# Performance work log

Measured on AMD Instinct MI355X. Metric: run time of the kernel, lower is better.

The kernel has to match this reference:

```python
import jax, jax.numpy as jnp
import numpy as np

DIM = 1024          # n_embd
NUM_EXPERTS = 8
TOP_K = 2
HIDDEN = 4 * DIM // TOP_K   # expert_hidden_dim = 2048
BS, SLEN = 1, 2048


def setup_inputs() -> dict:
    key = jax.random.key(0)
    k0, k1, k2, k3 = jax.random.split(key, 4)
    x = jax.random.normal(k0, (BS, SLEN, DIM), dtype=jnp.float32)
    gate_w = jax.random.normal(k1, (NUM_EXPERTS, DIM), dtype=jnp.float32) * 0.02
    w_up = jax.random.normal(k2, (NUM_EXPERTS, HIDDEN, DIM), dtype=jnp.float32) * 0.02
    w_down = jax.random.normal(k3, (NUM_EXPERTS, DIM, HIDDEN), dtype=jnp.float32) * 0.02
    expert_bias = jnp.zeros((NUM_EXPERTS,), dtype=jnp.float32)
    return {"x": x, "gate_w": gate_w, "w_up": w_up, "w_down": w_down,
            "expert_bias": expert_bias}


def _moe(x, gate_w, w_up, w_down, expert_bias):
    bs, slen, dim = x.shape
    xf = x.reshape(-1, dim)                       # (T, D)
    # Sigmoid router (scores in fp32, bias only affects selection, not weights)
    scores = jax.nn.sigmoid(xf @ gate_w.T)        # (T, E)
    biased = scores + expert_bias
    _, sel = jax.lax.top_k(biased, TOP_K)         # (T, K) expert ids, distinct per token
    top_scores = jnp.take_along_axis(scores, sel, axis=-1)  # (T, K)

    # Scatter/gather dispatch + grouped GEMM is mathematically equivalent to:
    #   out[t] = sum_k W_down[e_tk] @ relu(W_up[e_tk] @ (s_tk * x[t]))^2
    # Loop over the small fixed expert set via lax.scan; unassigned tokens
    # contribute exactly zero (relu(0)^2 = 0), honoring the routing sparsity.
    def body(acc, ew):
        e, wu, wd = ew
        # combined routing weight for this expert per token (at most one slot)
        w_t = jnp.sum(jnp.where(sel == e, top_scores, 0.0), axis=-1)  # (T,)
        xe = xf * w_t[:, None]                    # (T, D), zero for non-routed
        h = jnp.square(jax.nn.relu(xe @ wu.T))    # (T, H)  relu(x)^2 activation
        return acc + h @ wd.T, None

    out0 = jnp.zeros_like(xf)
    out, _ = jax.lax.scan(body, out0, (jnp.arange(NUM_EXPERTS), w_up, w_down))
    return out.reshape(bs, slen, dim)


def reference(x, gate_w, w_up, w_down, expert_bias):
    return _moe(x, gate_w, w_up, w_down, expert_bias)
```

## Files before the change

### kernel.cpp

```cpp
#include <hip/hip_runtime.h>
#include <cstdint>
#include <cstddef>

#define T_TOK 2048
#define DMODEL 1024
#define NEXP 8
#define HID 2048
#define DUMP_ID 4096

typedef __bf16 bf16x8 __attribute__((ext_vector_type(8)));
typedef float f32x4 __attribute__((ext_vector_type(4)));
typedef unsigned short u16;
typedef u16 u16x8 __attribute__((ext_vector_type(8)));

__device__ __forceinline__ u16 f2bf(float f) {
    union { float f; unsigned int u; } v; v.f = f;
    unsigned int u = v.u;
    unsigned int r = (u + 0x7FFFu + ((u >> 16) & 1u)) >> 16;
    return (u16)r;
}

__device__ __forceinline__ void gl2lds16(const void* g, void* l) {
    __builtin_amdgcn_global_load_lds(
        (const __attribute__((address_space(1))) void*)g,
        (__attribute__((address_space(3))) void*)l,
        16, 0, 0);
}

__global__ __launch_bounds__(256) void fused_pre(
    const float4* __restrict__ x4, const float4* __restrict__ gw4,
    const float* __restrict__ bias, ushort4* __restrict__ xb4,
    unsigned int* __restrict__ selpack, float* __restrict__ w2,
    unsigned int* __restrict__ xb_dump_row_u32) {
    const int b = blockIdx.x;
    const int tid = threadIdx.x;

    if (b == 256) {
        if (tid < DMODEL / 2) xb_dump_row_u32[tid] = 0;
        return;
    }
    const int wv = tid >> 6;
    const int lane = tid & 63;
    const int pair = b * 4 + wv;
    const int t0 = 2 * pair, t1 = t0 + 1;

    float acc0[NEXP], acc1[NEXP];
#pragma unroll
    for (int e = 0; e < NEXP; ++e) { acc0[e] = 0.f; acc1[e] = 0.f; }
#pragma unroll
    for (int j = 0; j < 4; ++j) {
        int i4 = lane + j * 64;
        float4 a0 = x4[t0 * 256 + i4];
        float4 a1 = x4[t1 * 256 + i4];
        ushort4 s0, s1;
        s0.x = f2bf(a0.x); s0.y = f2bf(a0.y); s0.z = f2bf(a0.z); s0.w = f2bf(a0.w);
        s1.x = f2bf(a1.x); s1.y = f2bf(a1.y); s1.z = f2bf(a1.z); s1.w = f2bf(a1.w);
        xb4[t0 * 256 + i4] = s0;
        xb4[t1 * 256 + i4] = s1;
#pragma unroll
        for (int e = 0; e < NEXP; ++e) {
            float4 g = gw4[e * 256 + i4];
            acc0[e] += a0.x * g.x + a0.y * g.y + a0.z * g.z + a0.w * g.w;
            acc1[e] += a1.x * g.x + a1.y * g.y + a1.z * g.z + a1.w * g.w;
        }
    }
#pragma unroll
    for (int e = 0; e < NEXP; ++e)
        for (int off = 32; off > 0; off >>= 1) {
            acc0[e] += __shfl_xor(acc0[e], off, 64);
            acc1[e] += __shfl_xor(acc1[e], off, 64);
        }
    if (lane == 0) {
#pragma unroll
        for (int tt = 0; tt < 2; ++tt) {
            int t = tt ? t1 : t0;
            float sc[NEXP], bi[NEXP];
#pragma unroll
            for (int e = 0; e < NEXP; ++e) {
                float a = tt ? acc1[e] : acc0[e];
                sc[e] = 1.f / (1.f + expf(-a));
                bi[e] = sc[e] + bias[e];
            }
            int e0 = 0;
            for (int e = 1; e < NEXP; ++e) if (bi[e] > bi[e0]) e0 = e;
            int e1 = -1;
            for (int e = 0; e < NEXP; ++e) {
                if (e == e0) continue;
                if (e1 < 0 || bi[e] > bi[e1]) e1 = e;
            }
            selpack[t] = (unsigned int)e0 | ((unsigned int)e1 << 8);
            w2[2 * t]     = sc[e0] * sc[e0];
            w2[2 * t + 1] = sc[e1] * sc[e1];
        }
    }
}

__global__ __launch_bounds__(256) void build_lists(
    const unsigned int* __restrict__ selpack, int* __restrict__ counts,
    int* __restrict__ list) {
    const int e = blockIdx.x;
    const int tid = threadIdx.x;
    const int lane = tid & 63;
    const int wv = tid >> 6;
    __shared__ int wsum[4];
    __shared__ int base;
    if (tid == 0) base = 0;
    __syncthreads();
    for (int tb = 0; tb < T_TOK; tb += 256) {
        int t = tb + tid;
        unsigned int sp = selpack[t];
        bool f1 = ((sp >> 8) & 255u) == (unsigned)e;
        bool f = ((sp & 255u) == (unsigned)e) | f1;
        int id = 2 * t + (f1 ? 1 : 0);
        unsigned long long m = __ballot(f);
        int pos = __popcll(m & ((1ull << lane) - 1ull));
        if (lane == 0) wsum[wv] = __popcll(m);
        __syncthreads();
        int woff = 0;
#pragma unroll
        for (int i = 0; i < 4; ++i) if (i < wv) woff += wsum[i];
        int bse = base;
        if (f) list[e * T_TOK + bse + woff + pos] = id;
        __syncthreads();
        if (tid == 0) base = bse + wsum[0] + wsum[1] + wsum[2] + wsum[3];
    }
    __syncthreads();
    int total = base;
    if (tid == 0) counts[e] = total;
    for (int i = total + tid; i < T_TOK; i += 256) list[e * T_TOK + i] = DUMP_ID;
}

template <int MODE>
__global__ __launch_bounds__(256, 2) void moe_gemm(
    const u16* __restrict__ Asrc, const int* __restrict__ list,
    const int* __restrict__ counts, const float* __restrict__ Ball32,
    const float* __restrict__ w2, u16* __restrict__ Hout,
    float* __restrict__ Pout) {
    constexpr int K   = (MODE == 0) ? DMODEL : HID;
    constexpr int NKT = K / 64;
    constexpr int NTN = ((MODE == 0) ? HID : DMODEL) / 128;
    constexpr int LOGNTN = (MODE == 0) ? 4 : 3;

    const int b = blockIdx.x;
    const int e = b & 7;
    const int rest = b >> 3;
    const int m0 = (rest >> LOGNTN) * 128;
    if (m0 >= counts[e]) return;
    const int n0 = (rest & (NTN - 1)) * 128;

    const int tid = threadIdx.x;
    const int lane = tid & 63;
    const int w = tid >> 6;

    __shared__ u16 As[128 * 64];
    __shared__ u16 Bs[128 * 64];

    const int* mylist = list + e * T_TOK + m0;
    const float* B32 = Ball32 + (size_t)e * HID * DMODEL;

    const u16* ap[4];
    const float4* bp[4];
    int bwr[4];
    const int c8 = tid & 7;
#pragma unroll
    for (int it = 0; it < 4; ++it) {
        int row = it * 32 + (tid >> 3);
        int gs = c8 ^ (row & 7);
        if (MODE == 0) {
            int id = mylist[row];
            ap[it] = Asrc + (size_t)(id >> 1) * K + gs * 8;
        } else {
            ap[it] = Asrc + (size_t)(e * T_TOK + m0 + row) * K + gs * 8;
        }
        bp[it] = (const float4*)(B32 + (size_t)(n0 + row) * K) + c8 * 2;
        bwr[it] = row * 64 + gs * 8;
    }

    const int wm = (w >> 1) * 64;
    const int wn = (w & 1) * 64;
    const int quad = lane >> 4;
    const int lrow = lane & 15;

    f32x4 acc[4][4];
#pragma unroll
    for (int i = 0; i < 4; ++i)
#pragma unroll
        for (int j = 0; j < 4; ++j) acc[i][j] = f32x4{0.f, 0.f, 0.f, 0.f};

    for (int kt = 0; kt < NKT; ++kt) {
#pragma unroll
        for (int it = 0; it < 4; ++it)
            gl2lds16(ap[it] + kt * 64, &As[(it * 256 + w * 64) * 8]);
        float4 bu[4][2];
#pragma unroll
        for (int it = 0; it < 4; ++it) {
            bu[it][0] = bp[it][kt * 16];
            bu[it][1] = bp[it][kt * 16 + 1];
        }
#pragma unroll
        for (int it = 0; it < 4; ++it) {
            u16x8 o;
            o[0] = f2bf(bu[it][0].x); o[1] = f2bf(bu[it][0].y);
            o[2] = f2bf(bu[it][0].z); o[3] = f2bf(bu[it][0].w);
            o[4] = f2bf(bu[it][1].x); o[5] = f2bf(bu[it][1].y);
            o[6] = f2bf(bu[it][1].z); o[7] = f2bf(bu[it][1].w);
            *(u16x8*)&Bs[bwr[it]] = o;
        }
        __syncthreads();
#pragma unroll
        for (int s = 0; s < 2; ++s) {
            const int q = s * 4 + quad;
            bf16x8 af[4], bfr[4];
#pragma unroll
            for (int i = 0; i < 4; ++i) {
                int ra = wm + i * 16 + lrow;
                int rb = wn + i * 16 + lrow;
                af[i]  = *(const bf16x8*)&As[ra * 64 + (q ^ (ra & 7)) * 8];
                bfr[i] = *(const bf16x8*)&Bs[rb * 64 + (q ^ (rb & 7)) * 8];
            }
#pragma unroll
            for (int i = 0; i < 4; ++i)
#pragma unroll
                for (int j = 0; j < 4; ++j)
                    acc[i][j] = __builtin_amdgcn_mfma_f32_16x16x32_bf16(
                        af[i], bfr[j], acc[i][j], 0, 0, 0);
        }
        __syncthreads();
    }

#pragma unroll
    for (int i = 0; i < 4; ++i) {
        int mbase = wm + i * 16 + (lane >> 4) * 4;
        int ids[4];
        float ww[4];
#pragma unroll
        for (int r = 0; r < 4; ++r) {
            ids[r] = mylist[mbase + r];
            if (MODE == 0) ww[r] = w2[ids[r]];
        }
#pragma unroll
        for (int j = 0; j < 4; ++j) {
            int n = n0 + wn + j * 16 + (lane & 15);
#pragma unroll
            for (int r = 0; r < 4; ++r) {
                float v = acc[i][j][r];
                if (MODE == 0) {
                    v = (v > 0.f) ? v * v * ww[r] : 0.f;
                    Hout[(size_t)(e * T_TOK + m0 + mbase + r) * HID + n] = f2bf(v);
                } else {
                    if (ids[r] != DUMP_ID)
                        Pout[(size_t)ids[r] * DMODEL + n] = v;
                }
            }
        }
    }
}

__global__ __launch_bounds__(256) void combine(
    const float4* __restrict__ part4, float4* __restrict__ out4) {
    int idx = blockIdx.x * 256 + threadIdx.x;
    int t = idx >> 8;
    int d4 = idx & 255;
    float4 p0 = part4[(size_t)(2 * t) * 256 + d4];
    float4 p1 = part4[(size_t)(2 * t + 1) * 256 + d4];
    float4 o;
    o.x = p0.x + p1.x; o.y = p0.y + p1.y;
    o.z = p0.z + p1.z; o.w = p0.w + p1.w;
    out4[idx] = o;
}

extern "C" void kernel_launch(void* const* d_in, const int* in_sizes, int n_in,
                              void* d_out, int out_size, void* d_ws, size_t ws_size,
                              hipStream_t stream) {
    const float* x      = (const float*)d_in[0];
    const float* gate_w = (const float*)d_in[1];
    const float* w_up   = (const float*)d_in[2];
    const float* w_down = (const float*)d_in[3];
    const float* bias   = (const float*)d_in[4];
    float* out = (float*)d_out;

    char* p = (char*)d_ws;
    int* counts = (int*)p;                 p += 256;
    int* list   = (int*)p;                 p += NEXP * T_TOK * 4;
    float* w2   = (float*)p;               p += 4104 * 4;
    unsigned int* selpack = (unsigned int*)p;  p += T_TOK * 4;
    u16* xb  = (u16*)p;  p += (size_t)(T_TOK + 1) * DMODEL * 2;
    u16* h   = (u16*)p;  p += (size_t)NEXP * T_TOK * HID * 2;
    float* part = (float*)p;  p += (size_t)2 * T_TOK * DMODEL * 4;

    fused_pre<<<257, 256, 0, stream>>>(
        (const float4*)x, (const float4*)gate_w, bias,
        (ushort4*)xb, selpack, w2,
        (unsigned int*)(xb + (size_t)T_TOK * DMODEL));

    build_lists<<<NEXP, 256, 0, stream>>>(selpack, counts, list);

    moe_gemm<0><<<16 * (HID / 128) * NEXP, 256, 0, stream>>>(
        xb, list, counts, w_up, w2, h, nullptr);

    moe_gemm<1><<<16 * (DMODEL / 128) * NEXP, 256, 0, stream>>>(
        h, list, counts, w_down, w2, nullptr, part);

    combine<<<T_TOK * DMODEL / 4 / 256, 256, 0, stream>>>(
        (const float4*)part, (float4*)out);
}
```

Before: 255.0 us.

## Software-pipeline grouped GEMM K-loop with multi-buffered LDS and register prefetch

Restructures the expert GEMM main loop into a two-stage-ahead software pipeline. A tiles go into a triple-buffered LDS ring via direct global-to-LDS loads, and B tiles are prefetched into alternating register sets before being converted to bf16 into double-buffered LDS. Explicit vmcnt waits and one barrier per step replace the two syncthreads per iteration. The goal is to hide global load latency behind the MFMA work, at the cost of more LDS (80KB) and more registers, which may lower occupancy.

```diff
diff --git a/kernel.cpp b/kernel.cpp
--- a/kernel.cpp
+++ b/kernel.cpp
@@ -26,6 +26,14 @@
         (__attribute__((address_space(3))) void*)l,
         16, 0, 0);
 }
+
+#define WAITV(N) asm volatile("s_waitcnt vmcnt(" #N ")" ::: "memory")
+#define LGKM0_BAR()                                            \
+    do {                                                       \
+        asm volatile("s_waitcnt lgkmcnt(0)" ::: "memory");     \
+        __builtin_amdgcn_s_barrier();                          \
+        __builtin_amdgcn_sched_barrier(0);                     \
+    } while (0)
 
 __global__ __launch_bounds__(256) void fused_pre(
     const float4* __restrict__ x4, const float4* __restrict__ gw4,
@@ -152,8 +160,8 @@
     const int lane = tid & 63;
     const int w = tid >> 6;
 
-    __shared__ u16 As[128 * 64];
-    __shared__ u16 Bs[128 * 64];
+    __shared__ u16 As[3][128 * 64];
+    __shared__ u16 Bs[2][128 * 64];
 
     const int* mylist = list + e * T_TOK + m0;
     const float* B32 = Ball32 + (size_t)e * HID * DMODEL;
@@ -187,26 +195,42 @@
 #pragma unroll
         for (int j = 0; j < 4; ++j) acc[i][j] = f32x4{0.f, 0.f, 0.f, 0.f};
 
-    for (int kt = 0; kt < NKT; ++kt) {
-#pragma unroll
-        for (int it = 0; it < 4; ++it)
-            gl2lds16(ap[it] + kt * 64, &As[(it * 256 + w * 64) * 8]);
-        float4 bu[4][2];
-#pragma unroll
-        for (int it = 0; it < 4; ++it) {
-            bu[it][0] = bp[it][kt * 16];
-            bu[it][1] = bp[it][kt * 16 + 1];
-        }
-#pragma unroll
-        for (int it = 0; it < 4; ++it) {
-            u16x8 o;
-            o[0] = f2bf(bu[it][0].x); o[1] = f2bf(bu[it][0].y);
-            o[2] = f2bf(bu[it][0].z); o[3] = f2bf(bu[it][0].w);
-            o[4] = f2bf(bu[it][1].x); o[5] = f2bf(bu[it][1].y);
-            o[6] = f2bf(bu[it][1].z); o[7] = f2bf(bu[it][1].w);
-            *(u16x8*)&Bs[bwr[it]] = o;
-        }
-        __syncthreads();
+    float4 buE[4][2], buO[4][2];
+
+#define ISSUE_A(KT)                                                          \
+    do {                                                                     \
+        u16* dst_ = &As[(KT) % 3][0];                                        \
+        _Pragma("unroll")                                                    \
+        for (int it_ = 0; it_ < 4; ++it_)                                    \
+            gl2lds16(ap[it_] + (KT) * 64, dst_ + (it_ * 256 + w * 64) * 8);  \
+    } while (0)
+
+#define LOAD_B(KT, BU)                                                       \
+    do {                                                                     \
+        _Pragma("unroll")                                                    \
+        for (int it_ = 0; it_ < 4; ++it_) {                                  \
+            BU[it_][0] = bp[it_][(KT) * 16];                                 \
+            BU[it_][1] = bp[it_][(KT) * 16 + 1];                             \
+        }                                                                    \
+    } while (0)
+
+#define WRITE_B(KT, BU)                                                      \
+    do {                                                                     \
+        u16* dst_ = &Bs[(KT) & 1][0];                                        \
+        _Pragma("unroll")                                                    \
+        for (int it_ = 0; it_ < 4; ++it_) {                                  \
+            u16x8 o_;                                                        \
+            o_[0] = f2bf(BU[it_][0].x); o_[1] = f2bf(BU[it_][0].y);          \
+            o_[2] = f2bf(BU[it_][0].z); o_[3] = f2bf(BU[it_][0].w);          \
+            o_[4] = f2bf(BU[it_][1].x); o_[5] = f2bf(BU[it_][1].y);          \
+            o_[6] = f2bf(BU[it_][1].z); o_[7] = f2bf(BU[it_][1].w);          \
+            *(u16x8*)(dst_ + bwr[it_]) = o_;                                 \
+        }                                                                    \
+    } while (0)
+
+    auto compute = [&](int kt) {
+        const u16* As_ = &As[kt % 3][0];
+        const u16* Bs_ = &Bs[kt & 1][0];
 #pragma unroll
         for (int s = 0; s < 2; ++s) {
             const int q = s * 4 + quad;
@@ -215,8 +239,8 @@
             for (int i = 0; i < 4; ++i) {
                 int ra = wm + i * 16 + lrow;
                 int rb = wn + i * 16 + lrow;
-                af[i]  = *(const bf16x8*)&As[ra * 64 + (q ^ (ra & 7)) * 8];
-                bfr[i] = *(const bf16x8*)&Bs[rb * 64 + (q ^ (rb & 7)) * 8];
+                af[i]  = *(const bf16x8*)(As_ + ra * 64 + (q ^ (ra & 7)) * 8);
+                bfr[i] = *(const bf16x8*)(Bs_ + rb * 64 + (q ^ (rb & 7)) * 8);
             }
 #pragma unroll
             for (int i = 0; i < 4; ++i)
@@ -225,8 +249,40 @@
                     acc[i][j] = __builtin_amdgcn_mfma_f32_16x16x32_bf16(
                         af[i], bfr[j], acc[i][j], 0, 0, 0);
         }
-        __syncthreads();
-    }
+    };
+
+    LOAD_B(0, buE);
+    ISSUE_A(0);
+    LOAD_B(1, buO);
+    ISSUE_A(1);
+    WAITV(12);
+    WRITE_B(0, buE);
+    LGKM0_BAR();
+
+    for (int kt = 0; kt < NKT; kt += 2) {
+        {
+            const bool i2 = (kt + 2 < NKT);
+            if (i2) { LOAD_B(kt + 2, buE); ISSUE_A(kt + 2); }
+            compute(kt);
+            if (i2) WAITV(16); else WAITV(4);
+            WRITE_B(kt + 1, buO);
+            if (i2) WAITV(12); else WAITV(0);
+            LGKM0_BAR();
+        }
+        {
+            const int k1 = kt + 1;
+            const bool i2 = (k1 + 2 < NKT);
+            if (i2) { LOAD_B(k1 + 2, buO); ISSUE_A(k1 + 2); }
+            compute(k1);
+            if (i2) WAITV(16); else WAITV(4);
+            if (k1 + 1 < NKT) WRITE_B(k1 + 1, buE);
+            if (i2) WAITV(12); else WAITV(0);
+            LGKM0_BAR();
+        }
+    }
+#undef ISSUE_A
+#undef LOAD_B
+#undef WRITE_B
 
 #pragma unroll
     for (int i = 0; i < 4; ++i) {
```

Measured after the change: 266.8 us. +4.6%, slower.

## Fuse all MoE stages into one persistent kernel with grid barriers

Applied to the files above, without the earlier changes.

Replaces the five separate launches (router/convert, list build, up GEMM, down GEMM, combine) with a single persistent kernel of 512 blocks. The stages are separated by atomic-counter grid barriers, and each GEMM stage loops over its tiles. This removes per-launch overhead and gaps between kernels. In exchange it adds a memset launch, spin-wait barriers, and reliance on all 512 blocks being co-resident. The static tile striding may also balance GEMM work less well than a full hardware-scheduled grid.

```diff
diff --git a/kernel.cpp b/kernel.cpp
--- a/kernel.cpp
+++ b/kernel.cpp
@@ -7,6 +7,7 @@
 #define NEXP 8
 #define HID 2048
 #define DUMP_ID 4096
+#define NBLK 512
 
 typedef __bf16 bf16x8 __attribute__((ext_vector_type(8)));
 typedef float f32x4 __attribute__((ext_vector_type(4)));
@@ -27,123 +28,33 @@
         16, 0, 0);
 }
 
-__global__ __launch_bounds__(256) void fused_pre(
-    const float4* __restrict__ x4, const float4* __restrict__ gw4,
-    const float* __restrict__ bias, ushort4* __restrict__ xb4,
-    unsigned int* __restrict__ selpack, float* __restrict__ w2,
-    unsigned int* __restrict__ xb_dump_row_u32) {
-    const int b = blockIdx.x;
-    const int tid = threadIdx.x;
-
-    if (b == 256) {
-        if (tid < DMODEL / 2) xb_dump_row_u32[tid] = 0;
-        return;
-    }
-    const int wv = tid >> 6;
-    const int lane = tid & 63;
-    const int pair = b * 4 + wv;
-    const int t0 = 2 * pair, t1 = t0 + 1;
-
-    float acc0[NEXP], acc1[NEXP];
-#pragma unroll
-    for (int e = 0; e < NEXP; ++e) { acc0[e] = 0.f; acc1[e] = 0.f; }
-#pragma unroll
-    for (int j = 0; j < 4; ++j) {
-        int i4 = lane + j * 64;
-        float4 a0 = x4[t0 * 256 + i4];
-        float4 a1 = x4[t1 * 256 + i4];
-        ushort4 s0, s1;
-        s0.x = f2bf(a0.x); s0.y = f2bf(a0.y); s0.z = f2bf(a0.z); s0.w = f2bf(a0.w);
-        s1.x = f2bf(a1.x); s1.y = f2bf(a1.y); s1.z = f2bf(a1.z); s1.w = f2bf(a1.w);
-        xb4[t0 * 256 + i4] = s0;
-        xb4[t1 * 256 + i4] = s1;
-#pragma unroll
-        for (int e = 0; e < NEXP; ++e) {
-            float4 g = gw4[e * 256 + i4];
-            acc0[e] += a0.x * g.x + a0.y * g.y + a0.z * g.z + a0.w * g.w;
-            acc1[e] += a1.x * g.x + a1.y * g.y + a1.z * g.z + a1.w * g.w;
-        }
-    }
-#pragma unroll
-    for (int e = 0; e < NEXP; ++e)
-        for (int off = 32; off > 0; off >>= 1) {
-            acc0[e] += __shfl_xor(acc0[e], off, 64);
-            acc1[e] += __shfl_xor(acc1[e], off, 64);
-        }
-    if (lane == 0) {
-#pragma unroll
-        for (int tt = 0; tt < 2; ++tt) {
-            int t = tt ? t1 : t0;
-            float sc[NEXP], bi[NEXP];
-#pragma unroll
-            for (int e = 0; e < NEXP; ++e) {
-                float a = tt ? acc1[e] : acc0[e];
-                sc[e] = 1.f / (1.f + expf(-a));
-                bi[e] = sc[e] + bias[e];
-            }
-            int e0 = 0;
-            for (int e = 1; e < NEXP; ++e) if (bi[e] > bi[e0]) e0 = e;
-            int e1 = -1;
-            for (int e = 0; e < NEXP; ++e) {
-                if (e == e0) continue;
-                if (e1 < 0 || bi[e] > bi[e1]) e1 = e;
-            }
-            selpack[t] = (unsigned int)e0 | ((unsigned int)e1 << 8);
-            w2[2 * t]     = sc[e0] * sc[e0];
-            w2[2 * t + 1] = sc[e1] * sc[e1];
-        }
-    }
-}
-
-__global__ __launch_bounds__(256) void build_lists(
-    const unsigned int* __restrict__ selpack, int* __restrict__ counts,
-    int* __restrict__ list) {
-    const int e = blockIdx.x;
-    const int tid = threadIdx.x;
-    const int lane = tid & 63;
-    const int wv = tid >> 6;
-    __shared__ int wsum[4];
-    __shared__ int base;
-    if (tid == 0) base = 0;
+__device__ __forceinline__ void gbar(int* bar, int idx) {
+    __threadfence();
     __syncthreads();
-    for (int tb = 0; tb < T_TOK; tb += 256) {
-        int t = tb + tid;
-        unsigned int sp = selpack[t];
-        bool f1 = ((sp >> 8) & 255u) == (unsigned)e;
-        bool f = ((sp & 255u) == (unsigned)e) | f1;
-        int id = 2 * t + (f1 ? 1 : 0);
-        unsigned long long m = __ballot(f);
-        int pos = __popcll(m & ((1ull << lane) - 1ull));
-        if (lane == 0) wsum[wv] = __popcll(m);
-        __syncthreads();
-        int woff = 0;
-#pragma unroll
-        for (int i = 0; i < 4; ++i) if (i < wv) woff += wsum[i];
-        int bse = base;
-        if (f) list[e * T_TOK + bse + woff + pos] = id;
-        __syncthreads();
-        if (tid == 0) base = bse + wsum[0] + wsum[1] + wsum[2] + wsum[3];
+    if (threadIdx.x == 0) {
+        atomicAdd(&bar[idx], 1);
+        while (atomicAdd(&bar[idx], 0) < NBLK)
+            __builtin_amdgcn_s_sleep(8);
     }
     __syncthreads();
-    int total = base;
-    if (tid == 0) counts[e] = total;
-    for (int i = total + tid; i < T_TOK; i += 256) list[e * T_TOK + i] = DUMP_ID;
+    __threadfence();
 }
 
 template <int MODE>
-__global__ __launch_bounds__(256, 2) void moe_gemm(
-    const u16* __restrict__ Asrc, const int* __restrict__ list,
-    const int* __restrict__ counts, const float* __restrict__ Ball32,
-    const float* __restrict__ w2, u16* __restrict__ Hout,
-    float* __restrict__ Pout) {
+__device__ void gemm_tile(int tix, const u16* __restrict__ Asrc,
+                          const int* __restrict__ list,
+                          const int* __restrict__ counts,
+                          const float* __restrict__ Ball32,
+                          const float* __restrict__ w2,
+                          u16* __restrict__ Hout, float* __restrict__ Pout,
+                          u16* As, u16* Bs) {
     constexpr int K   = (MODE == 0) ? DMODEL : HID;
     constexpr int NKT = K / 64;
     constexpr int NTN = ((MODE == 0) ? HID : DMODEL) / 128;
     constexpr int LOGNTN = (MODE == 0) ? 4 : 3;
 
-    const int b = blockIdx.x;
-    const int e = b & 7;
-    const int rest = b >> 3;
+    const int e = tix & 7;
+    const int rest = tix >> 3;
     const int m0 = (rest >> LOGNTN) * 128;
     if (m0 >= counts[e]) return;
     const int n0 = (rest & (NTN - 1)) * 128;
@@ -151,9 +62,6 @@
     const int tid = threadIdx.x;
     const int lane = tid & 63;
     const int w = tid >> 6;
-
-    __shared__ u16 As[128 * 64];
-    __shared__ u16 Bs[128 * 64];
 
     const int* mylist = list + e * T_TOK + m0;
     const float* B32 = Ball32 + (size_t)e * HID * DMODEL;
@@ -256,30 +164,151 @@
     }
 }
 
-__global__ __launch_bounds__(256) void combine(
-    const float4* __restrict__ part4, float4* __restrict__ out4) {
-    int idx = blockIdx.x * 256 + threadIdx.x;
-    int t = idx >> 8;
-    int d4 = idx & 255;
-    float4 p0 = part4[(size_t)(2 * t) * 256 + d4];
-    float4 p1 = part4[(size_t)(2 * t + 1) * 256 + d4];
-    float4 o;
-    o.x = p0.x + p1.x; o.y = p0.y + p1.y;
-    o.z = p0.z + p1.z; o.w = p0.w + p1.w;
-    out4[idx] = o;
+__global__ __launch_bounds__(256, 2) void moe_fused(
+    const float4* __restrict__ x4, const float4* __restrict__ gw4,
+    const float* __restrict__ bias,
+    u16* __restrict__ xb, unsigned int* __restrict__ selpack,
+    float* __restrict__ w2, int* __restrict__ counts, int* __restrict__ list,
+    const float* __restrict__ wu32, const float* __restrict__ wd32,
+    u16* __restrict__ h, float* __restrict__ part, float* __restrict__ out,
+    int* __restrict__ bar) {
+    const int b = blockIdx.x;
+    const int tid = threadIdx.x;
+
+    __shared__ u16 As[128 * 64];
+    __shared__ u16 Bs[128 * 64];
+    __shared__ int wsum[4];
+    __shared__ int sbase;
+
+    if (b < 256) {
+        ushort4* xb4 = (ushort4*)xb;
+        const int wv = tid >> 6;
+        const int lane = tid & 63;
+        const int pair = b * 4 + wv;
+        const int t0 = 2 * pair, t1 = t0 + 1;
+
+        float acc0[NEXP], acc1[NEXP];
+#pragma unroll
+        for (int e = 0; e < NEXP; ++e) { acc0[e] = 0.f; acc1[e] = 0.f; }
+#pragma unroll
+        for (int j = 0; j < 4; ++j) {
+            int i4 = lane + j * 64;
+            float4 a0 = x4[t0 * 256 + i4];
+            float4 a1 = x4[t1 * 256 + i4];
+            ushort4 s0, s1;
+            s0.x = f2bf(a0.x); s0.y = f2bf(a0.y); s0.z = f2bf(a0.z); s0.w = f2bf(a0.w);
+            s1.x = f2bf(a1.x); s1.y = f2bf(a1.y); s1.z = f2bf(a1.z); s1.w = f2bf(a1.w);
+            xb4[t0 * 256 + i4] = s0;
+            xb4[t1 * 256 + i4] = s1;
+#pragma unroll
+            for (int e = 0; e < NEXP; ++e) {
+                float4 g = gw4[e * 256 + i4];
+                acc0[e] += a0.x * g.x + a0.y * g.y + a0.z * g.z + a0.w * g.w;
+                acc1[e] += a1.x * g.x + a1.y * g.y + a1.z * g.z + a1.w * g.w;
+            }
+        }
+#pragma unroll
+        for (int e = 0; e < NEXP; ++e)
+            for (int off = 32; off > 0; off >>= 1) {
+                acc0[e] += __shfl_xor(acc0[e], off, 64);
+                acc1[e] += __shfl_xor(acc1[e], off, 64);
+            }
+        if (lane == 0) {
+#pragma unroll
+            for (int tt = 0; tt < 2; ++tt) {
+                int t = tt ? t1 : t0;
+                float sc[NEXP], bi[NEXP];
+#pragma unroll
+                for (int e = 0; e < NEXP; ++e) {
+                    float a = tt ? acc1[e] : acc0[e];
+                    sc[e] = 1.f / (1.f + expf(-a));
+                    bi[e] = sc[e] + bias[e];
+                }
+                int e0 = 0;
+                for (int e = 1; e < NEXP; ++e) if (bi[e] > bi[e0]) e0 = e;
+                int e1 = -1;
+                for (int e = 0; e < NEXP; ++e) {
+                    if (e == e0) continue;
+                    if (e1 < 0 || bi[e] > bi[e1]) e1 = e;
+                }
+                selpack[t] = (unsigned int)e0 | ((unsigned int)e1 << 8);
+                w2[2 * t]     = sc[e0] * sc[e0];
+                w2[2 * t + 1] = sc[e1] * sc[e1];
+            }
+        }
+    } else if (b == 256) {
+        unsigned int* xbdump = (unsigned int*)(xb + (size_t)T_TOK * DMODEL);
+        for (int i = tid; i < DMODEL / 2; i += 256) xbdump[i] = 0;
+    }
+    gbar(bar, 0);
+
+    if (b < NEXP) {
+        const int e = b;
+        const int lane = tid & 63;
+        const int wv = tid >> 6;
+        if (tid == 0) sbase = 0;
+        __syncthreads();
+        for (int tb = 0; tb < T_TOK; tb += 256) {
+            int t = tb + tid;
+            unsigned int sp = selpack[t];
+            bool f1 = ((sp >> 8) & 255u) == (unsigned)e;
+            bool f = ((sp & 255u) == (unsigned)e) | f1;
+            int id = 2 * t + (f1 ? 1 : 0);
+            unsigned long long m = __ballot(f);
+            int pos = __popcll(m & ((1ull << lane) - 1ull));
+            if (lane == 0) wsum[wv] = __popcll(m);
+            __syncthreads();
+            int woff = 0;
+#pragma unroll
+            for (int i = 0; i < 4; ++i) if (i < wv) woff += wsum[i];
+            int bse = sbase;
+            if (f) list[e * T_TOK + bse + woff + pos] = id;
+            __syncthreads();
+            if (tid == 0) sbase = bse + wsum[0] + wsum[1] + wsum[2] + wsum[3];
+        }
+        __syncthreads();
+        int total = sbase;
+        if (tid == 0) counts[e] = total;
+        for (int i = total + tid; i < T_TOK; i += 256) list[e * T_TOK + i] = DUMP_ID;
+    }
+    gbar(bar, 1);
+
+    for (int t = b; t < (T_TOK / 128) * (HID / 128) * NEXP; t += NBLK)
+        gemm_tile<0>(t, xb, list, counts, wu32, w2, h, nullptr, As, Bs);
+    gbar(bar, 2);
+
+    for (int t = b; t < (T_TOK / 128) * (DMODEL / 128) * NEXP; t += NBLK)
+        gemm_tile<1>(t, h, list, counts, wd32, w2, nullptr, part, As, Bs);
+    gbar(bar, 3);
+
+    {
+        const float4* p4 = (const float4*)part;
+        float4* o4 = (float4*)out;
+        for (int idx = b * 256 + tid; idx < T_TOK * DMODEL / 4; idx += NBLK * 256) {
+            int t = idx >> 8;
+            int d4 = idx & 255;
+            float4 p0 = p4[(size_t)(2 * t) * 256 + d4];
+            float4 p1 = p4[(size_t)(2 * t + 1) * 256 + d4];
+            float4 o;
+            o.x = p0.x + p1.x; o.y = p0.y + p1.y;
+            o.z = p0.z + p1.z; o.w = p0.w + p1.w;
+            o4[idx] = o;
+        }
+    }
 }
 
 extern "C" void kernel_launch(void* const* d_in, const int* in_sizes, int n_in,
                               void* d_out, int out_size, void* d_ws, size_t ws_size,
                               hipStream_t stream) {
-    const float* x      = (const float*)d_in[0];
-    const float* gate_w = (const float*)d_in[1];
-    const float* w_up   = (const float*)d_in[2];
-    const float* w_down = (const float*)d_in[3];
-    const float* bias   = (const float*)d_in[4];
+    const float4* x4  = (const float4*)d_in[0];
+    const float4* gw4 = (const float4*)d_in[1];
+    const float* wu32 = (const float*)d_in[2];
+    const float* wd32 = (const float*)d_in[3];
+    const float* bias = (const float*)d_in[4];
     float* out = (float*)d_out;
 
     char* p = (char*)d_ws;
+    int* bar    = (int*)p;                 p += 64;
     int* counts = (int*)p;                 p += 256;
     int* list   = (int*)p;                 p += NEXP * T_TOK * 4;
     float* w2   = (float*)p;               p += 4104 * 4;
@@ -288,19 +317,9 @@
     u16* h   = (u16*)p;  p += (size_t)NEXP * T_TOK * HID * 2;
     float* part = (float*)p;  p += (size_t)2 * T_TOK * DMODEL * 4;
 
-    fused_pre<<<257, 256, 0, stream>>>(
-        (const float4*)x, (const float4*)gate_w, bias,
-        (ushort4*)xb, selpack, w2,
-        (unsigned int*)(xb + (size_t)T_TOK * DMODEL));
-
-    build_lists<<<NEXP, 256, 0, stream>>>(selpack, counts, list);
-
-    moe_gemm<0><<<16 * (HID / 128) * NEXP, 256, 0, stream>>>(
-        xb, list, counts, w_up, w2, h, nullptr);
-
-    moe_gemm<1><<<16 * (DMODEL / 128) * NEXP, 256, 0, stream>>>(
-        h, list, counts, w_down, w2, nullptr, part);
-
-    combine<<<T_TOK * DMODEL / 4 / 256, 256, 0, stream>>>(
-        (const float4*)part, (float4*)out);
-}
+    hipMemsetAsync(bar, 0, 64, stream);
+
+    moe_fused<<<NBLK, 256, 0, stream>>>(
+        x4, gw4, bias, xb, selpack, w2, counts, list,
+        wu32, wd32, h, part, out, bar);
+}
```

New measurement: 711.1 us. 2.79x slower.
